# Kernel tuning notes

Measured on AMD Instinct MI355X. Metric: run time of the kernel, lower is better.

## Reference

```python
import jax, jax.numpy as jnp
import numpy as np

NTOKEN = 32000
NHID = 256
L = 128   # leaves per tree (power of 2 -> complete binary tree)
B = 512   # batch


def _postorder_perm(n_leaves):
    """Permutation mapping level-major node order -> stack-machine post-order."""
    levels = int(np.log2(n_leaves))
    sizes = [n_leaves >> l for l in range(levels + 1)]
    offsets = np.concatenate([[0], np.cumsum(sizes)])[:-1]
    order = []

    def rec(l, j):
        if l > 0:
            rec(l - 1, 2 * j)
            rec(l - 1, 2 * j + 1)
        order.append(int(offsets[l] + j))

    rec(levels, 0)
    return np.asarray(order, dtype=np.int32)


def _lstm_combine(hL, cL, hR, cR, W, b):
    # Same math as LSTMOp.forward: Linear(2H -> 5H), 5-way chunk, gates.
    g = jnp.concatenate([hL, hR], axis=-1) @ W + b  # [..., 5H]
    i_, f1_, f2_, o_, u_ = jnp.split(g, 5, axis=-1)
    c = (jax.nn.sigmoid(i_) * jnp.tanh(u_)
         + jax.nn.sigmoid(f1_) * cL
         + jax.nn.sigmoid(f2_) * cR)
    h = jax.nn.sigmoid(o_) * jnp.tanh(c)
    return h, c


def setup_inputs() -> dict:
    key = jax.random.key(0)
    k1, k2, k3, k4 = jax.random.split(key, 4)
    leaf_tokens = jax.random.randint(k1, (L, B), 0, NTOKEN)
    emb = 0.02 * jax.random.normal(k2, (NTOKEN, NHID), dtype=jnp.float32)
    emb_aux = 0.02 * jax.random.normal(k3, (NTOKEN, NHID), dtype=jnp.float32)
    W = jax.random.normal(k4, (2 * NHID, 5 * NHID), dtype=jnp.float32) / np.sqrt(2 * NHID)
    b = jnp.zeros((5 * NHID,), dtype=jnp.float32)
    return {"leaf_tokens": leaf_tokens, "emb": emb, "emb_aux": emb_aux, "W": W, "b": b}


def reference(leaf_tokens, emb, emb_aux, W, b):
    n_leaves, batch = leaf_tokens.shape
    leaves = emb[leaf_tokens]          # [L, B, H]
    leaves_aux = emb_aux[leaf_tokens]  # [L, B, H]

    # Level-by-level combine over the complete binary tree (vectorized across
    # pairs and batch); leaves enter the op as (h, c=0) exactly as in torch.
    h = leaves
    c = jnp.zeros_like(h)
    per_level_h = [h]
    while h.shape[0] > 1:
        h, c = _lstm_combine(h[0::2], c[0::2], h[1::2], c[1::2], W, b)
        per_level_h.append(h)

    all_h = jnp.concatenate(per_level_h, axis=0)        # [2L-1, B, H] level-major
    perm = jnp.asarray(_postorder_perm(n_leaves))
    internal_states = all_h[perm]                       # stack-machine post-order
    root = h[0]                                         # [B, H]

    # All trees have identical (full) length -> masks are all True.
    leaves_mask = jnp.ones((n_leaves, batch), dtype=bool)
    internal_mask = jnp.ones((2 * n_leaves - 1, batch), dtype=bool)
    return root, internal_states, internal_mask, leaves, leaves_aux, leaves_mask
```

## Files before the change

### kernel.cpp

```cpp
#include <hip/hip_runtime.h>
#include <hip/hip_bf16.h>
#include <hip/hip_fp16.h>
#include <cstdint>
#include <cstddef>

#define H 256
#define L 128
#define B 512
#define LEVELS 7
#define BH (B * H)

#define OFF_ROOT 0
#define OFF_INT (B * H)
#define OFF_IMASK (OFF_INT + 255 * BH)
#define OFF_LEAVES (OFF_IMASK + 255 * B)
#define OFF_LAUX (OFF_LEAVES + L * BH)
#define OFF_LMASK (OFF_LAUX + L * BH)

typedef unsigned short u16;
typedef __attribute__((ext_vector_type(8))) _Float16 half8;
typedef __attribute__((ext_vector_type(4))) float f32x4;
typedef __attribute__((ext_vector_type(4))) u16 u16x4;
typedef __attribute__((ext_vector_type(16))) float f32x16;

#if __has_builtin(__builtin_amdgcn_exp2f)
#define EXP2(x) __builtin_amdgcn_exp2f(x)
#else
#define EXP2(x) exp2f(x)
#endif
#if __has_builtin(__builtin_amdgcn_rcpf)
#define RCP(x) __builtin_amdgcn_rcpf(x)
#else
#define RCP(x) (1.0f / (x))
#endif

__device__ __forceinline__ float fsigm(float x) {
    return RCP(1.0f + EXP2(-1.442695041f * x));
}
__device__ __forceinline__ float ftanh(float x) {
    return 1.0f - 2.0f * RCP(1.0f + EXP2(2.885390082f * x));
}


__device__ __forceinline__ int postorder_pos(int level, int j) {
    int start = 0;
    for (int k = level; k <= LEVELS; ++k) {
        if ((j >> (k - level)) & 1) start += (2 << k) - 1;
    }
    return start + (2 << level) - 2;
}

__device__ __forceinline__ u16 f2h(float x) {
    _Float16 h = (_Float16)x;
    u16 u;
    __builtin_memcpy(&u, &h, 2);
    return u;
}
__device__ __forceinline__ float h2f(u16 u) {
    _Float16 h;
    __builtin_memcpy(&h, &u, 2);
    return (float)h;
}

__device__ __forceinline__ void gload16(const void* g, const void* l) {
    __builtin_amdgcn_global_load_lds(
        (const __attribute__((address_space(1))) void*)g,
        (__attribute__((address_space(3))) void*)l, 16, 0, 0);
}

__global__ __launch_bounds__(256) void gather_kernel(
    const int* __restrict__ tok, const float* __restrict__ emb,
    const float* __restrict__ emb_aux, float* __restrict__ out,
    u16* __restrict__ spLeaf) {
    int row = blockIdx.x * 4 + (threadIdx.x >> 6);
    int f4i = threadIdx.x & 63;
    int l = row >> 9, b = row & 511;
    int t = tok[row];
    f32x4 e = *(reinterpret_cast<const f32x4*>(emb + (size_t)t * H) + f4i);
    f32x4 ea = *(reinterpret_cast<const f32x4*>(emb_aux + (size_t)t * H) + f4i);
    __builtin_nontemporal_store(
        e, reinterpret_cast<f32x4*>(out + OFF_LEAVES) + (size_t)row * 64 + f4i);
    __builtin_nontemporal_store(
        ea, reinterpret_cast<f32x4*>(out + OFF_LAUX) + (size_t)row * 64 + f4i);
    int pp = postorder_pos(0, l);
    __builtin_nontemporal_store(
        e, reinterpret_cast<f32x4*>(out + OFF_INT + (size_t)pp * BH +
                                    (size_t)b * H) +
               f4i);
    int ko = f4i >> 2;
    int lanep = (b & 31) + 32 * ((f4i >> 1) & 1);
    int elem0 = 4 * (f4i & 1);
    u16x4 hv;
    hv.x = f2h(e.x); hv.y = f2h(e.y); hv.z = f2h(e.z); hv.w = f2h(e.w);
    u16* np = spLeaf + (size_t)l * BH +
              (size_t)(((b >> 5) * 16 + ko) * 512 + lanep * 8 + elem0);
    *reinterpret_cast<u16x4*>(np) = hv;
}

__global__ __launch_bounds__(256) void wpack_kernel(const float* __restrict__ W,
                                                    u16* __restrict__ wp,
                                                    float* __restrict__ out) {
    int q = blockIdx.x * 256 + threadIdx.x;
    int k = q / 1280, col = q - k * 1280;
    int gate = col >> 8, hc = col & 255;
    int hcb = hc >> 5, cl = hc & 31;
    int kb = k >> 5, klr = k & 31;
    int ks = klr >> 4, oct = (klr >> 3) & 1, elem = klr & 7;
    size_t off = ((size_t)(hcb * 16 + kb) * 10 + gate * 2 + ks) * 512 +
                 (cl + 32 * oct) * 8 + elem;
    wp[off] = f2h(W[q]);
    if (q < 255 * B) __builtin_nontemporal_store(1.0f, out + OFF_IMASK + q);
    if (q < L * B) __builtin_nontemporal_store(1.0f, out + OFF_LMASK + q);
}

__global__ __launch_bounds__(128) void lstm_level(
    const u16* __restrict__ wp, const float* __restrict__ bias,
    float* __restrict__ out, u16* __restrict__ spA, u16* __restrict__ cAll,
    int lev) {
    __shared__ __align__(16) u16 Wld[4][10 * 512];

    const int tid = threadIdx.x;
    const int lane = tid & 63;
    const int wm = tid >> 6;
    const int l31 = lane & 31;
    const int lh = lane >> 5;

    const int j = blockIdx.x;
    const int p = j >> 5;
    const int b0c = (j >> 3) & 3;
    const int hcb = j & 7;

    const int b0 = b0c * 128;
    const int hc0 = hcb * 32;
    const int cb = 256 - (256 >> (lev - 1));
    const int nid = 256 - (256 >> lev) + p;

    const u16* sL = spA + (size_t)(cb + 2 * p) * BH;
    const u16* sR = sL + BH;

    f32x16 acc[2][5];
#pragma unroll
    for (int nf = 0; nf < 5; ++nf) {
        float bv = bias[nf * H + hc0 + l31];
        f32x16 v;
#pragma unroll
        for (int r = 0; r < 16; ++r) v[r] = bv;
        acc[0][nf] = v;
        acc[1][nf] = v;
    }

    half8 Af[4][2][2];

    auto stage = [&](int buf, int kb) {
        const u16* wsrc = wp + ((size_t)(hcb * 16 + kb) * 10) * 512;
#pragma unroll
        for (int i = 0; i < 5; ++i) {
            int t = 5 * wm + i;
            gload16(wsrc + t * 512 + lane * 8, &Wld[buf][t * 512]);
        }
        const u16* pl = (kb < 8) ? sL : sR;
#pragma unroll
        for (int mf = 0; mf < 2; ++mf)
#pragma unroll
            for (int ks = 0; ks < 2; ++ks) {
                int T = ((b0 >> 5) + 2 * wm + mf) * 16 + (kb & 7) * 2 + ks;
                Af[buf][mf][ks] = *reinterpret_cast<const half8*>(
                    pl + (size_t)T * 512 + lane * 8);
            }
    };

    stage(0, 0);
    stage(1, 1);
#pragma unroll
    for (int kb = 0; kb < 16; ++kb) {
        const int cur = kb & 3;
        if (kb < 14) {
            stage((kb + 2) & 3, kb + 2);
            asm volatile("s_waitcnt vmcnt(18)" ::: "memory");
        } else if (kb == 14) {
            asm volatile("s_waitcnt vmcnt(9)" ::: "memory");
        } else {
            asm volatile("s_waitcnt vmcnt(0)" ::: "memory");
        }
        __builtin_amdgcn_s_barrier();
        __builtin_amdgcn_sched_barrier(0);
#pragma unroll
        for (int ks = 0; ks < 2; ++ks)
#pragma unroll
            for (int nf = 0; nf < 5; ++nf) {
                half8 bf = *reinterpret_cast<const half8*>(
                    &Wld[cur][(nf * 2 + ks) * 512 + lane * 8]);
                acc[0][nf] = __builtin_amdgcn_mfma_f32_32x32x16_f16(
                    Af[cur][0][ks], bf, acc[0][nf], 0, 0, 0);
                acc[1][nf] = __builtin_amdgcn_mfma_f32_32x32x16_f16(
                    Af[cur][1][ks], bf, acc[1][nf], 0, 0, 0);
            }
    }

    const int pout = postorder_pos(lev, p);
    float* __restrict__ hout = out + OFF_INT + (size_t)pout * BH;
    u16* __restrict__ cob = cAll + (size_t)(nid - 128) * BH;
    const u16* cLf =
        (lev >= 2) ? cAll + (size_t)(cb + 2 * p - 128) * BH : nullptr;
    const u16* cRf = cLf ? cLf + BH : nullptr;
    u16* __restrict__ soH = (lev < 7) ? spA + (size_t)nid * BH : nullptr;
    const int hc = hc0 + l31;
    const int kop = hcb * 2 + (l31 >> 4);
    const int lpp = 32 * ((l31 >> 3) & 1);
    const int elp = l31 & 7;

#pragma unroll
    for (int mf = 0; mf < 2; ++mf) {
        const int g = (b0 >> 5) + 2 * wm + mf;
        const size_t fbase =
            (((size_t)(g * 8 + hcb) * 8) + lh * 4) * 128 + l31 * 4;
#pragma unroll
        for (int q = 0; q < 4; ++q) {
            float cl4[4] = {0.f, 0.f, 0.f, 0.f};
            float cr4[4] = {0.f, 0.f, 0.f, 0.f};
            if (cLf) {
                u16x4 a = *reinterpret_cast<const u16x4*>(cLf + fbase + q * 128);
                u16x4 bq = *reinterpret_cast<const u16x4*>(cRf + fbase + q * 128);
                cl4[0] = h2f(a.x); cl4[1] = h2f(a.y);
                cl4[2] = h2f(a.z); cl4[3] = h2f(a.w);
                cr4[0] = h2f(bq.x); cr4[1] = h2f(bq.y);
                cr4[2] = h2f(bq.z); cr4[3] = h2f(bq.w);
            }
            u16x4 co4;
#pragma unroll
            for (int e = 0; e < 4; ++e) {
                const int r = 4 * q + e;
                float ig = acc[mf][0][r], f1 = acc[mf][1][r];
                float f2 = acc[mf][2][r], og = acc[mf][3][r];
                float ug = acc[mf][4][r];
                float c = fsigm(ig) * ftanh(ug) + fsigm(f1) * cl4[e] +
                          fsigm(f2) * cr4[e];
                float hval = fsigm(og) * ftanh(c);
                co4[e] = f2h(c);
                const int b = b0 + 64 * wm + 32 * mf + 4 * lh + e + 8 * q;
                __builtin_nontemporal_store(hval, hout + (size_t)b * H + hc);
                if (soH)
                    soH[(size_t)((b >> 5) * 16 + kop) * 512 +
                        (size_t)((b & 31) + lpp) * 8 + elp] = f2h(hval);
                if (lev == LEVELS)
                    __builtin_nontemporal_store(
                        hval, out + OFF_ROOT + (size_t)b * H + hc);
            }
            *reinterpret_cast<u16x4*>(cob + fbase + q * 128) = co4;
        }
    }
}

extern "C" void kernel_launch(void* const* d_in, const int* in_sizes, int n_in,
                              void* d_out, int out_size, void* d_ws,
                              size_t ws_size, hipStream_t stream) {
    const int* tok = (const int*)d_in[0];
    const float* emb = (const float*)d_in[1];
    const float* emb_aux = (const float*)d_in[2];
    const float* W = (const float*)d_in[3];
    const float* bias = (const float*)d_in[4];
    float* out = (float*)d_out;

    u16* wp = (u16*)d_ws;
    u16* spA = wp + (size_t)655360;
    u16* cAll = spA + (size_t)254 * BH;

    hipLaunchKernelGGL(wpack_kernel, dim3(2560), dim3(256), 0, stream, W, wp,
                       out);
    hipLaunchKernelGGL(gather_kernel, dim3(L * B / 4), dim3(256), 0, stream,
                       tok, emb, emb_aux, out, spA);

    for (int level = 1; level <= LEVELS; ++level) {
        int units = 32 * (L >> level);
        hipLaunchKernelGGL(lstm_level, dim3(units), dim3(128), 0, stream, wp,
                           bias, out, spA, cAll, level);
    }
}
```

Baseline: 277.3 us.

## Fuse tree levels four through seven into one dataflow kernel with flags

Replaces the four separate launches for the upper tree levels with a single persistent kernel. Each block spins on per-node/batch-chunk counters in global memory until its two child nodes have been fully produced, then computes and releases its own counter. This removes kernel launch gaps and the tail idle time between small levels, at the cost of spin-waiting and a dependence on all 480 blocks being co-resident (checked through an occupancy query, with the per-level launches kept as a fallback).

```diff
diff --git a/kernel.cpp b/kernel.cpp
--- a/kernel.cpp
+++ b/kernel.cpp
@@ -99,7 +99,8 @@
 
 __global__ __launch_bounds__(256) void wpack_kernel(const float* __restrict__ W,
                                                     u16* __restrict__ wp,
-                                                    float* __restrict__ out) {
+                                                    float* __restrict__ out,
+                                                    int* __restrict__ flags) {
     int q = blockIdx.x * 256 + threadIdx.x;
     int k = q / 1280, col = q - k * 1280;
     int gate = col >> 8, hc = col & 255;
@@ -111,25 +112,14 @@
     wp[off] = f2h(W[q]);
     if (q < 255 * B) __builtin_nontemporal_store(1.0f, out + OFF_IMASK + q);
     if (q < L * B) __builtin_nontemporal_store(1.0f, out + OFF_LMASK + q);
-}
-
-__global__ __launch_bounds__(128) void lstm_level(
-    const u16* __restrict__ wp, const float* __restrict__ bias,
-    float* __restrict__ out, u16* __restrict__ spA, u16* __restrict__ cAll,
-    int lev) {
-    __shared__ __align__(16) u16 Wld[4][10 * 512];
-
-    const int tid = threadIdx.x;
-    const int lane = tid & 63;
-    const int wm = tid >> 6;
-    const int l31 = lane & 31;
-    const int lh = lane >> 5;
-
-    const int j = blockIdx.x;
-    const int p = j >> 5;
-    const int b0c = (j >> 3) & 3;
-    const int hcb = j & 7;
-
+    if (q < 64) flags[q] = 0;
+}
+
+__device__ __forceinline__ void run_unit(
+    int lev, int p, int b0c, int hcb, const u16* __restrict__ wp,
+    const float* __restrict__ bias, float* __restrict__ out,
+    u16* __restrict__ spA, u16* __restrict__ cAll, u16 (*Wld)[10 * 512],
+    int lane, int wm, int l31, int lh) {
     const int b0 = b0c * 128;
     const int hc0 = hcb * 32;
     const int cb = 256 - (256 >> (lev - 1));
@@ -251,6 +241,58 @@
     }
 }
 
+__global__ __launch_bounds__(128) void lstm_level(
+    const u16* __restrict__ wp, const float* __restrict__ bias,
+    float* __restrict__ out, u16* __restrict__ spA, u16* __restrict__ cAll,
+    int lev) {
+    __shared__ __align__(16) u16 Wld[4][10 * 512];
+    const int tid = threadIdx.x;
+    const int j = blockIdx.x;
+    run_unit(lev, j >> 5, (j >> 3) & 3, j & 7, wp, bias, out, spA, cAll, Wld,
+             tid & 63, tid >> 6, tid & 31 & 63, (tid & 63) >> 5);
+}
+
+__global__ __launch_bounds__(128) void tree_tail(
+    const u16* __restrict__ wp, const float* __restrict__ bias,
+    float* __restrict__ out, u16* __restrict__ spA, u16* __restrict__ cAll,
+    int* __restrict__ flags) {
+    __shared__ __align__(16) u16 Wld[4][10 * 512];
+    const int tid = threadIdx.x;
+    const int lane = tid & 63;
+
+    int u = blockIdx.x, lev, rem;
+    if (u < 256)      { lev = 4; rem = u; }
+    else if (u < 384) { lev = 5; rem = u - 256; }
+    else if (u < 448) { lev = 6; rem = u - 384; }
+    else              { lev = 7; rem = u - 448; }
+    const int p = rem >> 5;
+    const int b0c = (rem >> 3) & 3;
+    const int hcb = rem & 7;
+
+    if (lev >= 5) {
+        const int cb = 256 - (256 >> (lev - 1));
+        const int f0 = (cb + 2 * p - 240) * 4 + b0c;
+        while (__hip_atomic_load(&flags[f0], __ATOMIC_ACQUIRE,
+                                 __HIP_MEMORY_SCOPE_AGENT) < 8 ||
+               __hip_atomic_load(&flags[f0 + 4], __ATOMIC_ACQUIRE,
+                                 __HIP_MEMORY_SCOPE_AGENT) < 8)
+            __builtin_amdgcn_s_sleep(4);
+    }
+
+    run_unit(lev, p, b0c, hcb, wp, bias, out, spA, cAll, Wld, lane, tid >> 6,
+             lane & 31, lane >> 5);
+
+    if (lev < 7) {
+        const int nid = 256 - (256 >> lev) + p;
+        __threadfence();
+        __syncthreads();
+        if (tid == 0)
+            __hip_atomic_fetch_add(&flags[(nid - 240) * 4 + b0c], 1,
+                                   __ATOMIC_RELEASE,
+                                   __HIP_MEMORY_SCOPE_AGENT);
+    }
+}
+
 extern "C" void kernel_launch(void* const* d_in, const int* in_sizes, int n_in,
                               void* d_out, int out_size, void* d_ws,
                               size_t ws_size, hipStream_t stream) {
@@ -264,15 +306,33 @@
     u16* wp = (u16*)d_ws;
     u16* spA = wp + (size_t)655360;
     u16* cAll = spA + (size_t)254 * BH;
+    int* flags = (int*)(cAll + (size_t)127 * BH);
 
     hipLaunchKernelGGL(wpack_kernel, dim3(2560), dim3(256), 0, stream, W, wp,
-                       out);
+                       out, flags);
     hipLaunchKernelGGL(gather_kernel, dim3(L * B / 4), dim3(256), 0, stream,
                        tok, emb, emb_aux, out, spA);
 
-    for (int level = 1; level <= LEVELS; ++level) {
+    for (int level = 1; level <= 3; ++level) {
         int units = 32 * (L >> level);
         hipLaunchKernelGGL(lstm_level, dim3(units), dim3(128), 0, stream, wp,
                            bias, out, spA, cAll, level);
     }
-}
+
+    int maxb = 0, ncu = 256, dev = 0;
+    (void)hipGetDevice(&dev);
+    (void)hipDeviceGetAttribute(&ncu, hipDeviceAttributeMultiprocessorCount,
+                                dev);
+    (void)hipOccupancyMaxActiveBlocksPerMultiprocessor(&maxb, tree_tail, 128,
+                                                       0);
+    if (maxb * ncu >= 480) {
+        hipLaunchKernelGGL(tree_tail, dim3(480), dim3(128), 0, stream, wp,
+                           bias, out, spA, cAll, flags);
+    } else {
+        for (int level = 4; level <= LEVELS; ++level) {
+            int units = 32 * (L >> level);
+            hipLaunchKernelGGL(lstm_level, dim3(units), dim3(128), 0, stream,
+                               wp, bias, out, spA, cAll, level);
+        }
+    }
+}
```

After: 277.9 us. About the same (+0.2%).
